# Kernel optimization log

Measured on AMD Instinct MI355X. Metric: run time of the kernel, lower is better.

The kernel has to match this reference:

```python
import jax, jax.numpy as jnp
import numpy as np

EMBED_DIM = 1024
NUM_HEADS = 16
HEAD_DIM = EMBED_DIM // NUM_HEADS


def setup_inputs() -> dict:
    key = jax.random.key(0)
    ks = jax.random.split(key, 9)
    B, N, C = 4, 2048, EMBED_DIM
    scale = 1.0 / np.sqrt(C)
    x = jax.random.normal(ks[0], (B, N, C), dtype=jnp.float32)
    Wq = jax.random.normal(ks[1], (C, C), dtype=jnp.float32) * scale
    bq = jax.random.normal(ks[2], (C,), dtype=jnp.float32) * 0.01
    Wk = jax.random.normal(ks[3], (C, C), dtype=jnp.float32) * scale
    bk = jax.random.normal(ks[4], (C,), dtype=jnp.float32) * 0.01
    Wv = jax.random.normal(ks[5], (C, C), dtype=jnp.float32) * scale
    bv = jax.random.normal(ks[6], (C,), dtype=jnp.float32) * 0.01
    Wo = jax.random.normal(ks[7], (C, C), dtype=jnp.float32) * scale
    bo = jax.random.normal(ks[8], (C,), dtype=jnp.float32) * 0.01
    return {"x": x, "Wq": Wq, "bq": bq, "Wk": Wk, "bk": bk,
            "Wv": Wv, "bv": bv, "Wo": Wo, "bo": bo}


def reference(x, Wq, bq, Wk, bk, Wv, bv, Wo, bo):
    B, N, C = x.shape
    H, D = NUM_HEADS, HEAD_DIM
    # linear projections (weights stored as [in, out])
    Q = (x @ Wq + bq).reshape(B, N, H, D).transpose(0, 2, 1, 3)  # [B,H,N,D]
    K = (x @ Wk + bk).reshape(B, N, H, D).transpose(0, 2, 1, 3)
    V = (x @ Wv + bv).reshape(B, N, H, D).transpose(0, 2, 1, 3)
    scores = jnp.einsum('bhqd,bhkd->bhqk', Q, K) / jnp.sqrt(jnp.float32(D))
    attn = jax.nn.softmax(scores, axis=-1)
    out = jnp.einsum('bhqk,bhkd->bhqd', attn, V)  # [B,H,N,D]
    out = out.transpose(0, 2, 1, 3).reshape(B, N, C)
    return out @ Wo + bo
```

## Files before the change

kernel.cpp:

```cpp
#include <hip/hip_runtime.h>
#include <hip/hip_bf16.h>
#include <cstdint>


typedef __attribute__((ext_vector_type(8))) short short8;
typedef __attribute__((ext_vector_type(4))) float floatx4;

__device__ __forceinline__ unsigned short f2bf(float f) {
  unsigned u = __float_as_uint(f);
  unsigned r = u + 0x7fffu + ((u >> 16) & 1u);
  return (unsigned short)(r >> 16);
}

__device__ __forceinline__ void async16(const void* g, void* l) {
  __builtin_amdgcn_global_load_lds(
      (__attribute__((address_space(1))) void*)(void*)(uintptr_t)g,
      (__attribute__((address_space(3))) void*)l, 16, 0, 0);
}

__global__ __launch_bounds__(256) void cvt_kernel(const float* __restrict__ in,
                                                  unsigned short* __restrict__ out) {
  int i = (blockIdx.x * 256 + threadIdx.x) * 4;
  float4 v = *(const float4*)(in + i);
  ushort4 o;
  o.x = f2bf(v.x); o.y = f2bf(v.y); o.z = f2bf(v.z); o.w = f2bf(v.w);
  *(ushort4*)(out + i) = o;
}

__global__ __launch_bounds__(256) void trans_w(
    const float* __restrict__ W0, const float* __restrict__ W1,
    const float* __restrict__ W2, const float* __restrict__ W3,
    unsigned short* __restrict__ T0, unsigned short* __restrict__ T1,
    unsigned short* __restrict__ T2, unsigned short* __restrict__ T3) {
  const float* W = blockIdx.z == 0 ? W0 : blockIdx.z == 1 ? W1 : blockIdx.z == 2 ? W2 : W3;
  unsigned short* T = blockIdx.z == 0 ? T0 : blockIdx.z == 1 ? T1 : blockIdx.z == 2 ? T2 : T3;
  __shared__ float t[32][33];
  int tx = threadIdx.x, ty = threadIdx.y;
  int bx = blockIdx.x * 32, by = blockIdx.y * 32;
#pragma unroll
  for (int i = 0; i < 4; ++i)
    t[ty + i * 8][tx] = W[(size_t)(by + ty + i * 8) * 1024 + bx + tx];
  __syncthreads();
#pragma unroll
  for (int i = 0; i < 4; ++i)
    T[(size_t)(bx + ty + i * 8) * 1024 + by + tx] = f2bf(t[tx][ty + i * 8]);
}

__global__ __launch_bounds__(256) void gemm_qkv(
    const unsigned short* __restrict__ A, const unsigned short* __restrict__ BT,
    const float* __restrict__ bq, const float* __restrict__ bk,
    const float* __restrict__ bv,
    unsigned short* __restrict__ Qo, unsigned short* __restrict__ Ko,
    unsigned short* __restrict__ Vo) {
  constexpr int Kd = 1024;
  __shared__ unsigned short As[128 * 32];
  __shared__ unsigned short Bs[128 * 32];
  const int tid = threadIdx.x;
  const int wave = tid >> 6, lane = tid & 63;
  const int quad = lane >> 4, l16 = lane & 15;
  const int wm = (wave & 1) * 64, wn = (wave >> 1) * 64;
  const int m0 = blockIdx.x * 128, n0 = blockIdx.y * 128;
  const int mid = blockIdx.y >> 3;
  const float* bias = mid == 0 ? bq : mid == 1 ? bk : bv;
  unsigned short* outp = mid == 0 ? Qo : mid == 1 ? Ko : Vo;
  const float scale = mid == 0 ? 0.125f : 1.0f;

  floatx4 acc[4][4] = {};
  const unsigned short* Ag = A + (size_t)m0 * Kd;
  const unsigned short* Bg = BT + (size_t)n0 * Kd;

  for (int k0 = 0; k0 < Kd; k0 += 32) {
    __syncthreads();
#pragma unroll
    for (int p = 0; p < 2; ++p) {
      int c = wave * 128 + p * 64 + lane;
      int row = c >> 2, kp = (c & 3) * 8;
      async16(Ag + (size_t)row * Kd + k0 + kp, (char*)As + (size_t)(wave * 128 + p * 64) * 16);
      async16(Bg + (size_t)row * Kd + k0 + kp, (char*)Bs + (size_t)(wave * 128 + p * 64) * 16);
    }
    __syncthreads();
    short8 a[4], b[4];
#pragma unroll
    for (int i = 0; i < 4; ++i) {
      a[i] = *(const short8*)(As + (wm + i * 16 + l16) * 32 + quad * 8);
      b[i] = *(const short8*)(Bs + (wn + i * 16 + l16) * 32 + quad * 8);
    }
#pragma unroll
    for (int i = 0; i < 4; ++i)
#pragma unroll
      for (int j = 0; j < 4; ++j)
        acc[i][j] = __builtin_amdgcn_mfma_f32_16x16x32_bf16(a[i], b[j], acc[i][j], 0, 0, 0);
  }

#pragma unroll
  for (int j = 0; j < 4; ++j) {
    int gcol = n0 + wn + j * 16 + l16;
    int cn = gcol & 1023;
    float bb = bias[cn];
    int h = cn >> 6, d = cn & 63;
#pragma unroll
    for (int i = 0; i < 4; ++i) {
      int rbase = m0 + wm + i * 16 + quad * 4;
#pragma unroll
      for (int r = 0; r < 4; ++r) {
        int row = rbase + r;
        unsigned short hv = f2bf((acc[i][j][r] + bb) * scale);
        int bi = row >> 11, ni = row & 2047;
        size_t bh = (size_t)bi * 16 + h;
        if (mid == 2) {
          int nt = d >> 4, vl = d & 15;
          int kq = ni >> 5, vq = (ni & 31) >> 3, vj = ni & 7;
          Vo[((bh * 64 + kq) * 4 + nt) * 512 + vq * 128 + vl * 8 + vj] = hv;
        } else {
          int kfg = ni >> 4, tl = ni & 15;
          int kk = d >> 5, dq = (d & 31) >> 3, dj = d & 7;
          outp[((bh * 128 + kfg) * 2 + kk) * 512 + dq * 128 + tl * 8 + dj] = hv;
        }
      }
    }
  }
}

__global__ __launch_bounds__(256) void attn_kernel(
    const unsigned short* __restrict__ Qs, const unsigned short* __restrict__ Ksw,
    const unsigned short* __restrict__ Vsw, unsigned short* __restrict__ O) {
  __shared__ __align__(16) unsigned short Ps[4 * 32 * 40];

  const int tid = threadIdx.x, wave = tid >> 6, lane = tid & 63;
  const int quad = lane >> 4, l16 = lane & 15;
  int blk = blockIdx.x;
  int xcd = blk & 7, slot = blk >> 3;
  int qb = slot >> 3, bh = (slot & 7) * 8 + xcd;

  short8 aq[2][2];
#pragma unroll
  for (int rt = 0; rt < 2; ++rt)
#pragma unroll
    for (int kk = 0; kk < 2; ++kk)
      aq[rt][kk] = *(const short8*)(Qs +
          (((size_t)bh * 128 + qb * 8 + wave * 2 + rt) * 2 + kk) * 512 + lane * 8);

  short8 ones;
#pragma unroll
  for (int i = 0; i < 8; ++i) ones[i] = (short)0x3F80;

  floatx4 acc_o[2][4] = {};
  floatx4 acc_l[2] = {};
  const float LOG2E = 1.44269504088896f;
  const float MSUB = 17.3123404906676f;
  unsigned short* Pw = Ps + wave * 1280;

  const unsigned short* Kbh = Ksw + (size_t)bh * 128 * 2 * 512;
  const unsigned short* Vbh = Vsw + (size_t)bh * 64 * 4 * 512;

  for (int kt = 0; kt < 64; ++kt) {
    short8 kf[2][2];
#pragma unroll
    for (int ct = 0; ct < 2; ++ct)
#pragma unroll
      for (int kk = 0; kk < 2; ++kk)
        kf[ct][kk] = *(const short8*)(Kbh + ((size_t)(kt * 2 + ct) * 2 + kk) * 512 + lane * 8);
    short8 vf[4];
#pragma unroll
    for (int nt = 0; nt < 4; ++nt)
      vf[nt] = *(const short8*)(Vbh + ((size_t)kt * 4 + nt) * 512 + lane * 8);

    floatx4 sacc[2][2] = {};
#pragma unroll
    for (int kk = 0; kk < 2; ++kk)
#pragma unroll
      for (int ct = 0; ct < 2; ++ct)
#pragma unroll
        for (int rt = 0; rt < 2; ++rt)
          sacc[rt][ct] = __builtin_amdgcn_mfma_f32_16x16x32_bf16(aq[rt][kk], kf[ct][kk], sacc[rt][ct], 0, 0, 0);

#pragma unroll
    for (int rt = 0; rt < 2; ++rt)
#pragma unroll
      for (int ct = 0; ct < 2; ++ct)
#pragma unroll
        for (int r = 0; r < 4; ++r) {
          float pv = exp2f(fmaf(sacc[rt][ct][r], LOG2E, -MSUB));
          Pw[(rt * 16 + quad * 4 + r) * 40 + ct * 16 + l16] =
              (unsigned short)(__float_as_uint(pv) >> 16);
        }
#pragma unroll
    for (int rt = 0; rt < 2; ++rt) {
      short8 ap = *(const short8*)(Pw + (rt * 16 + l16) * 40 + quad * 8);
      acc_l[rt] = __builtin_amdgcn_mfma_f32_16x16x32_bf16(ap, ones, acc_l[rt], 0, 0, 0);
#pragma unroll
      for (int nt = 0; nt < 4; ++nt)
        acc_o[rt][nt] = __builtin_amdgcn_mfma_f32_16x16x32_bf16(ap, vf[nt], acc_o[rt][nt], 0, 0, 0);
    }
  }

  const int b = bh >> 4, h = bh & 15;
#pragma unroll
  for (int rt = 0; rt < 2; ++rt)
#pragma unroll
    for (int r = 0; r < 4; ++r) {
      float linv = 1.0f / acc_l[rt][r];
      int row = qb * 128 + wave * 32 + rt * 16 + quad * 4 + r;
#pragma unroll
      for (int nt = 0; nt < 4; ++nt) {
        int col = h * 64 + nt * 16 + l16;
        O[((size_t)b * 2048 + row) * 1024 + col] = f2bf(acc_o[rt][nt][r] * linv);
      }
    }
}

__global__ __launch_bounds__(256) void gemm_out(
    const unsigned short* __restrict__ A, const unsigned short* __restrict__ BT,
    const float* __restrict__ bias, float* __restrict__ of) {
  constexpr int Kd = 1024;
  __shared__ unsigned short As[128 * 32];
  __shared__ unsigned short Bs[128 * 32];
  const int tid = threadIdx.x;
  const int wave = tid >> 6, lane = tid & 63;
  const int quad = lane >> 4, l16 = lane & 15;
  const int wm = (wave & 1) * 64, wn = (wave >> 1) * 64;
  const int m0 = blockIdx.x * 128, n0 = blockIdx.y * 128;

  floatx4 acc[4][4] = {};
  const unsigned short* Ag = A + (size_t)m0 * Kd;
  const unsigned short* Bg = BT + (size_t)n0 * Kd;

  for (int k0 = 0; k0 < Kd; k0 += 32) {
    __syncthreads();
#pragma unroll
    for (int p = 0; p < 2; ++p) {
      int c = wave * 128 + p * 64 + lane;
      int row = c >> 2, kp = (c & 3) * 8;
      async16(Ag + (size_t)row * Kd + k0 + kp, (char*)As + (size_t)(wave * 128 + p * 64) * 16);
      async16(Bg + (size_t)row * Kd + k0 + kp, (char*)Bs + (size_t)(wave * 128 + p * 64) * 16);
    }
    __syncthreads();
    short8 a[4], b[4];
#pragma unroll
    for (int i = 0; i < 4; ++i) {
      a[i] = *(const short8*)(As + (wm + i * 16 + l16) * 32 + quad * 8);
      b[i] = *(const short8*)(Bs + (wn + i * 16 + l16) * 32 + quad * 8);
    }
#pragma unroll
    for (int i = 0; i < 4; ++i)
#pragma unroll
      for (int j = 0; j < 4; ++j)
        acc[i][j] = __builtin_amdgcn_mfma_f32_16x16x32_bf16(a[i], b[j], acc[i][j], 0, 0, 0);
  }

#pragma unroll
  for (int j = 0; j < 4; ++j) {
    int col = n0 + wn + j * 16 + l16;
    float bb = bias[col];
#pragma unroll
    for (int i = 0; i < 4; ++i) {
      int rbase = m0 + wm + i * 16 + quad * 4;
#pragma unroll
      for (int r = 0; r < 4; ++r)
        of[(size_t)(rbase + r) * 1024 + col] = acc[i][j][r] + bb;
    }
  }
}

extern "C" void kernel_launch(void* const* d_in, const int* in_sizes, int n_in,
                              void* d_out, int out_size, void* d_ws, size_t ws_size,
                              hipStream_t stream) {
  const float* x  = (const float*)d_in[0];
  const float* Wq = (const float*)d_in[1];
  const float* bq = (const float*)d_in[2];
  const float* Wk = (const float*)d_in[3];
  const float* bk = (const float*)d_in[4];
  const float* Wv = (const float*)d_in[5];
  const float* bv = (const float*)d_in[6];
  const float* Wo = (const float*)d_in[7];
  const float* bo = (const float*)d_in[8];

  char* ws = (char*)d_ws;
  unsigned short* xb  = (unsigned short*)(ws);
  unsigned short* wqt = (unsigned short*)(ws + (16u << 20));
  unsigned short* wkt = (unsigned short*)(ws + (18u << 20));
  unsigned short* wvt = (unsigned short*)(ws + (20u << 20));
  unsigned short* wot = (unsigned short*)(ws + (22u << 20));
  unsigned short* Qb  = (unsigned short*)(ws + (24u << 20));
  unsigned short* Kb  = (unsigned short*)(ws + (40u << 20));
  unsigned short* Vtb = (unsigned short*)(ws + (56u << 20));
  unsigned short* Ob  = (unsigned short*)(ws + (72u << 20));

  cvt_kernel<<<dim3(8192), dim3(256), 0, stream>>>(x, xb);
  trans_w<<<dim3(32, 32, 4), dim3(32, 8), 0, stream>>>(Wq, Wk, Wv, Wo, wqt, wkt, wvt, wot);
  gemm_qkv<<<dim3(64, 24), 256, 0, stream>>>(xb, wqt, bq, bk, bv, Qb, Kb, Vtb);
  attn_kernel<<<dim3(1024), 256, 0, stream>>>(Qb, Kb, Vtb, Ob);
  gemm_out<<<dim3(64, 8), 256, 0, stream>>>(Ob, wot, bo, (float*)d_out);
}
```

Baseline: 324.7 us.

## Split attention key range across wave pairs and fold log2e into Q scale

The attention kernel now runs twice as many blocks with 64 query rows each. Each pair of waves splits the 64 key tiles in half, and the partial output and row-sum accumulators are combined through shared memory at the end. The log2e factor moves into the Q projection scale, so the exp step becomes a subtract plus a raw exp2 builtin. Two P values are packed into one 32-bit LDS store with a perm instruction, which needs V's key order permuted to match. This is meant to add parallelism and occupancy and to cut ALU work in the softmax loop, at the cost of an extra reduction and two block barriers.

Measured after the change: 303.8 us. -6.5%, faster.

```diff
diff --git a/kernel.cpp b/kernel.cpp
--- a/kernel.cpp
+++ b/kernel.cpp
@@ -5,6 +5,12 @@
 
 typedef __attribute__((ext_vector_type(8))) short short8;
 typedef __attribute__((ext_vector_type(4))) float floatx4;
+
+#if __has_builtin(__builtin_amdgcn_exp2f)
+#define EXP2F(x) __builtin_amdgcn_exp2f(x)
+#else
+#define EXP2F(x) __expf((x) * 0.6931471805599453f)
+#endif
 
 __device__ __forceinline__ unsigned short f2bf(float f) {
   unsigned u = __float_as_uint(f);
@@ -62,8 +68,7 @@
   const int m0 = blockIdx.x * 128, n0 = blockIdx.y * 128;
   const int mid = blockIdx.y >> 3;
   const float* bias = mid == 0 ? bq : mid == 1 ? bk : bv;
-  unsigned short* outp = mid == 0 ? Qo : mid == 1 ? Ko : Vo;
-  const float scale = mid == 0 ? 0.125f : 1.0f;
+  const float scale = mid == 0 ? 0.180336880021082f : 1.0f;
 
   floatx4 acc[4][4] = {};
   const unsigned short* Ag = A + (size_t)m0 * Kd;
@@ -109,11 +114,13 @@
         size_t bh = (size_t)bi * 16 + h;
         if (mid == 2) {
           int nt = d >> 4, vl = d & 15;
-          int kq = ni >> 5, vq = (ni & 31) >> 3, vj = ni & 7;
-          Vo[((bh * 64 + kq) * 4 + nt) * 512 + vq * 128 + vl * 8 + vj] = hv;
+          int kq = ni >> 5, jk = ni & 31;
+          int pos = ((jk & 15) << 1) | (jk >> 4);
+          Vo[((bh * 64 + kq) * 4 + nt) * 512 + (pos >> 3) * 128 + vl * 8 + (pos & 7)] = hv;
         } else {
           int kfg = ni >> 4, tl = ni & 15;
           int kk = d >> 5, dq = (d & 31) >> 3, dj = d & 7;
+          unsigned short* outp = mid == 0 ? Qo : Ko;
           outp[((bh * 128 + kfg) * 2 + kk) * 512 + dq * 128 + tl * 8 + dj] = hv;
         }
       }
@@ -124,13 +131,16 @@
 __global__ __launch_bounds__(256) void attn_kernel(
     const unsigned short* __restrict__ Qs, const unsigned short* __restrict__ Ksw,
     const unsigned short* __restrict__ Vsw, unsigned short* __restrict__ O) {
-  __shared__ __align__(16) unsigned short Ps[4 * 32 * 40];
+  __shared__ __align__(16) char smem[17664];
 
   const int tid = threadIdx.x, wave = tid >> 6, lane = tid & 63;
   const int quad = lane >> 4, l16 = lane & 15;
+  const int wk = wave & 1, wqi = wave >> 1;
   int blk = blockIdx.x;
   int xcd = blk & 7, slot = blk >> 3;
-  int qb = slot >> 3, bh = (slot & 7) * 8 + xcd;
+  int bh = (slot & 7) * 8 + xcd, qb = slot >> 3;
+
+  unsigned short* Pw = (unsigned short*)smem + wave * 1280;
 
   short8 aq[2][2];
 #pragma unroll
@@ -138,7 +148,7 @@
 #pragma unroll
     for (int kk = 0; kk < 2; ++kk)
       aq[rt][kk] = *(const short8*)(Qs +
-          (((size_t)bh * 128 + qb * 8 + wave * 2 + rt) * 2 + kk) * 512 + lane * 8);
+          (((size_t)bh * 128 + qb * 4 + wqi * 2 + rt) * 2 + kk) * 512 + lane * 8);
 
   short8 ones;
 #pragma unroll
@@ -146,14 +156,13 @@
 
   floatx4 acc_o[2][4] = {};
   floatx4 acc_l[2] = {};
-  const float LOG2E = 1.44269504088896f;
-  const float MSUB = 17.3123404906676f;
-  unsigned short* Pw = Ps + wave * 1280;
+  const float MSUB = 17.3123404906675611f;
 
   const unsigned short* Kbh = Ksw + (size_t)bh * 128 * 2 * 512;
   const unsigned short* Vbh = Vsw + (size_t)bh * 64 * 4 * 512;
 
-  for (int kt = 0; kt < 64; ++kt) {
+  for (int kti = 0; kti < 32; ++kti) {
+    const int kt = wk * 32 + kti;
     short8 kf[2][2];
 #pragma unroll
     for (int ct = 0; ct < 2; ++ct)
@@ -177,13 +186,12 @@
 #pragma unroll
     for (int rt = 0; rt < 2; ++rt)
 #pragma unroll
-      for (int ct = 0; ct < 2; ++ct)
-#pragma unroll
-        for (int r = 0; r < 4; ++r) {
-          float pv = exp2f(fmaf(sacc[rt][ct][r], LOG2E, -MSUB));
-          Pw[(rt * 16 + quad * 4 + r) * 40 + ct * 16 + l16] =
-              (unsigned short)(__float_as_uint(pv) >> 16);
-        }
+      for (int r = 0; r < 4; ++r) {
+        float pe = EXP2F(sacc[rt][0][r] - MSUB);
+        float po = EXP2F(sacc[rt][1][r] - MSUB);
+        unsigned pk = __builtin_amdgcn_perm(__float_as_uint(po), __float_as_uint(pe), 0x07060302u);
+        ((unsigned*)(Pw + (rt * 16 + quad * 4 + r) * 40))[l16] = pk;
+      }
 #pragma unroll
     for (int rt = 0; rt < 2; ++rt) {
       short8 ap = *(const short8*)(Pw + (rt * 16 + l16) * 40 + quad * 8);
@@ -194,19 +202,38 @@
     }
   }
 
-  const int b = bh >> 4, h = bh & 15;
-#pragma unroll
-  for (int rt = 0; rt < 2; ++rt)
-#pragma unroll
-    for (int r = 0; r < 4; ++r) {
-      float linv = 1.0f / acc_l[rt][r];
-      int row = qb * 128 + wave * 32 + rt * 16 + quad * 4 + r;
-#pragma unroll
-      for (int nt = 0; nt < 4; ++nt) {
-        int col = h * 64 + nt * 16 + l16;
-        O[((size_t)b * 2048 + row) * 1024 + col] = f2bf(acc_o[rt][nt][r] * linv);
+  float* buf = (float*)smem + wqi * 2176;
+  float* lbuf = (float*)(smem + 17408);
+  __syncthreads();
+  if (wk == 1) {
+#pragma unroll
+    for (int rt = 0; rt < 2; ++rt)
+#pragma unroll
+      for (int r = 0; r < 4; ++r) {
+        int row = rt * 16 + quad * 4 + r;
+#pragma unroll
+        for (int nt = 0; nt < 4; ++nt)
+          buf[row * 68 + nt * 16 + l16] = acc_o[rt][nt][r];
+        if (l16 == 0) lbuf[wqi * 32 + row] = acc_l[rt][r];
       }
-    }
+  }
+  __syncthreads();
+  if (wk == 0) {
+    const int b = bh >> 4, h = bh & 15;
+#pragma unroll
+    for (int rt = 0; rt < 2; ++rt)
+#pragma unroll
+      for (int r = 0; r < 4; ++r) {
+        int row = rt * 16 + quad * 4 + r;
+        float linv = 1.0f / (acc_l[rt][r] + lbuf[wqi * 32 + row]);
+        int grow = qb * 64 + wqi * 32 + row;
+#pragma unroll
+        for (int nt = 0; nt < 4; ++nt) {
+          float v = (acc_o[rt][nt][r] + buf[row * 68 + nt * 16 + l16]) * linv;
+          O[((size_t)b * 2048 + grow) * 1024 + h * 64 + nt * 16 + l16] = f2bf(v);
+        }
+      }
+  }
 }
 
 __global__ __launch_bounds__(256) void gemm_out(
@@ -289,6 +316,6 @@
   cvt_kernel<<<dim3(8192), dim3(256), 0, stream>>>(x, xb);
   trans_w<<<dim3(32, 32, 4), dim3(32, 8), 0, stream>>>(Wq, Wk, Wv, Wo, wqt, wkt, wvt, wot);
   gemm_qkv<<<dim3(64, 24), 256, 0, stream>>>(xb, wqt, bq, bk, bv, Qb, Kb, Vtb);
-  attn_kernel<<<dim3(1024), 256, 0, stream>>>(Qb, Kb, Vtb, Ob);
+  attn_kernel<<<dim3(2048), 256, 0, stream>>>(Qb, Kb, Vtb, Ob);
   gemm_out<<<dim3(64, 8), 256, 0, stream>>>(Ob, wot, bo, (float*)d_out);
 }
```
